# Performance work log

Hardware: AMD Instinct MI355X
Metric: run time of the kernel (lower is better)

The kernel has to match this reference:

```python
import jax, jax.numpy as jnp
import numpy as np

N_NODES = 100000
N_EDGES = 1600000
D_IN = 512
D_HID = 128
N_CLASSES = 100


def _gcn_norm(edge_index, n_nodes):
    # Add self loops and compute symmetric normalization D^{-1/2} (A+I) D^{-1/2}
    sl = jnp.arange(n_nodes, dtype=edge_index.dtype)
    src = jnp.concatenate([edge_index[0], sl])
    dst = jnp.concatenate([edge_index[1], sl])
    deg = jax.ops.segment_sum(jnp.ones_like(dst, dtype=jnp.float32), dst,
                              num_segments=n_nodes)
    dinv = jnp.where(deg > 0, jax.lax.rsqrt(deg), 0.0)
    norm = dinv[src] * dinv[dst]  # [E + N]
    return src, dst, norm


def _gcn_layer(x, W, b, src, dst, norm, n_nodes):
    h = x @ W                                  # [N, d_out] (transform first, like PyG GCNConv)
    msg = h[src] * norm[:, None]               # [E+N, d_out] gather + scale
    out = jax.ops.segment_sum(msg, dst, num_segments=n_nodes)  # scatter-add
    return out + b


def setup_inputs() -> dict:
    key = jax.random.key(0)
    ks = jax.random.split(key, 6)
    x = jax.random.normal(ks[0], (N_NODES, D_IN), dtype=jnp.float32)
    edge_index = jax.random.randint(ks[1], (2, N_EDGES), 0, N_NODES, dtype=jnp.int64)
    W1 = jax.random.normal(ks[2], (D_IN, D_HID), dtype=jnp.float32) * (1.0 / np.sqrt(D_IN))
    b1 = jnp.zeros((D_HID,), dtype=jnp.float32)
    W2 = jax.random.normal(ks[3], (D_HID, N_CLASSES), dtype=jnp.float32) * (1.0 / np.sqrt(D_HID))
    b2 = jnp.zeros((N_CLASSES,), dtype=jnp.float32)
    return {"x": x, "edge_index": edge_index, "W1": W1, "b1": b1, "W2": W2, "b2": b2}


def reference(x, edge_index, W1, b1, W2, b2):
    n_nodes = x.shape[0]
    src, dst, norm = _gcn_norm(edge_index, n_nodes)
    h = jax.nn.relu(_gcn_layer(x, W1, b1, src, dst, norm, n_nodes))
    logits = _gcn_layer(h, W2, b2, src, dst, norm, n_nodes)
    return jax.nn.log_softmax(logits, axis=-1)
```

## Files before the change

### kernel.cpp

```cpp
#include <hip/hip_runtime.h>
#include <math.h>

typedef __attribute__((ext_vector_type(8))) short short8;
typedef __attribute__((ext_vector_type(4))) float f32x4;
typedef _Float16 half8 __attribute__((ext_vector_type(8)));
typedef __fp16 fp16x2 __attribute__((ext_vector_type(2)));
typedef unsigned int uint;

__device__ inline uint f2bf(float f) {
    uint u = __float_as_uint(f);
    return (u + 0x7fffu + ((u >> 16) & 1u)) >> 16;
}
__device__ inline uint pack2(float lo, float hi) { return f2bf(lo) | (f2bf(hi) << 16); }
__device__ inline float bflo(uint u) { return __uint_as_float(u << 16); }
__device__ inline float bfhi(uint u) { return __uint_as_float(u & 0xffff0000u); }
__device__ inline uint cvtpk(float lo, float hi) {
    uint r;
    asm("v_cvt_pk_bf16_f32 %0, %1, %2" : "=v"(r) : "v"(lo), "v"(hi));
    return r;
}
__device__ inline uint pkh(float lo, float hi) {
    union { fp16x2 h; uint u; } c;
    c.h = __builtin_amdgcn_cvt_pkrtz(lo, hi);
    return c.u;
}
__device__ inline void gload16(const void* g, void* l) {
    __builtin_amdgcn_global_load_lds(
        (const __attribute__((address_space(1))) void*)g,
        (__attribute__((address_space(3))) void*)l, 16, 0, 0);
}

__global__ void k_prep(const int* __restrict__ dst, int E, int nbE, int* __restrict__ cnt,
                       const float* __restrict__ W1, ushort* __restrict__ w1frag,
                       const float* __restrict__ W2, const float* __restrict__ b2,
                       ushort* __restrict__ w2frag, float* __restrict__ b2pad) {
    int bid = blockIdx.x;
    if (bid < nbE) {
        int i = bid * 256 + threadIdx.x;
        if (i < E) atomicAdd(&cnt[dst[i]], 1);
        return;
    }
    bid -= nbE;
    if (bid < 32) {
        int tid = bid * 256 + threadIdx.x;
        int ks = tid >> 9;
        int t = (tid >> 6) & 7;
        int l = tid & 63;
        int kbase = ks * 32 + (l >> 4) * 8;
        int c = t * 16 + (l & 15);
#pragma unroll
        for (int j = 0; j < 8; j++) {
            float v = W1[(size_t)(kbase + j) * 128 + c];
            union { _Float16 h; ushort u; } cv;
            cv.h = (_Float16)v;
            w1frag[(size_t)tid * 8 + j] = cv.u;
        }
        return;
    }
    bid -= 32;
    {
        int tid = bid * 256 + threadIdx.x;
        if (tid < 1792) {
            int q = tid / 448;
            int t = (tid >> 6) % 7;
            int l = tid & 63;
            int kbase = q * 32 + (l >> 4) * 8;
            int c = t * 16 + (l & 15);
#pragma unroll
            for (int j = 0; j < 8; j++) {
                float v = (c < 100) ? W2[(kbase + j) * 100 + c] : 0.f;
                w2frag[(size_t)tid * 8 + j] = (ushort)f2bf(v);
            }
        } else if (tid < 1792 + 112) {
            int c = tid - 1792;
            b2pad[c] = (c < 100) ? b2[c] : -1e30f;
        }
    }
}

__global__ __launch_bounds__(512) void k_scan1(const int* __restrict__ cnt, int* __restrict__ rp,
                                               int* __restrict__ partials, float* __restrict__ dinv,
                                               int N) {
    __shared__ int s[512];
    int i = blockIdx.x * 512 + threadIdx.x;
    int v = (i < N) ? cnt[i] : 0;
    if (i < N) dinv[i] = rsqrtf((float)(v + 1));
    s[threadIdx.x] = v;
    __syncthreads();
    for (int d = 1; d < 512; d <<= 1) {
        int t = (threadIdx.x >= d) ? s[threadIdx.x - d] : 0;
        __syncthreads();
        s[threadIdx.x] += t;
        __syncthreads();
    }
    if (i < N) rp[i] = s[threadIdx.x] - v;
    if (threadIdx.x == 511) partials[blockIdx.x] = s[511];
}

__global__ __launch_bounds__(512) void k_scan3(int* __restrict__ rp, const int* __restrict__ partials,
                                               int N, int E) {
    __shared__ int sw[8];
    int bid = blockIdx.x, tid = threadIdx.x;
    int acc = 0;
    for (int i = tid; i < bid; i += 512) acc += partials[i];
#pragma unroll
    for (int d = 32; d > 0; d >>= 1) acc += __shfl_xor(acc, d, 64);
    if ((tid & 63) == 0) sw[tid >> 6] = acc;
    __syncthreads();
    int tot = 0;
#pragma unroll
    for (int w = 0; w < 8; w++) tot += sw[w];
    int i = bid * 512 + tid;
    if (i < N) rp[i] += tot;
    if (i == 0) rp[N] = E;
}

__global__ __launch_bounds__(512) void k_fillgemm1(const int* __restrict__ src, const int* __restrict__ dst,
                                                   int E, int nbF, const int* __restrict__ rp,
                                                   int* __restrict__ cursor, const float* __restrict__ dinv,
                                                   float2* __restrict__ colw,
                                                   const float* __restrict__ x,
                                                   const uint4* __restrict__ w1f,
                                                   uint* __restrict__ h1, int N) {
    __shared__ __align__(16) char lds[49152];
    if (blockIdx.x < nbF) {
        int i = blockIdx.x * 512 + threadIdx.x;
        if (i < E) {
            int d = dst[i];
            int s = src[i];
            int pos = rp[d] + atomicAdd(&cursor[d], 1);
            colw[pos] = make_float2(__int_as_float(s), dinv[s]);
        }
        return;
    }
    int tid = threadIdx.x, wv = tid >> 6, l = tid & 63;
    int cl = l & 15, kg = l >> 4;
    int row0 = (blockIdx.x - nbF) * 64;
    int rq = wv & 3, chalf = wv >> 2;

    int xr = tid >> 3, xs = tid & 7;
    int xrg = row0 + xr; if (xrg >= N) xrg = N - 1;
    const float* xsrc = x + (size_t)xrg * 512 + xs * 8;

    auto stageB = [&](int c) {
        char* bbase = lds + 16384 + (c & 1) * 16384;
        const char* bsrc = (const char*)w1f + (size_t)c * 16384;
#pragma unroll
        for (int i = 0; i < 2; i++) {
            int s = i * 512 + tid;
            gload16(bsrc + (size_t)s * 16, bbase + (size_t)(s - l) * 16);
        }
    };

    float4 f0, f1;
    auto loadx = [&](int c) {
        const float* p = xsrc + c * 64;
        f0 = *(const float4*)p;
        f1 = *(const float4*)(p + 4);
    };
    auto writex = [&](int c) {
        char* xb = lds + (c & 1) * 8192;
        uint4 v;
        v.x = pkh(f0.x, f0.y);
        v.y = pkh(f0.z, f0.w);
        v.z = pkh(f1.x, f1.y);
        v.w = pkh(f1.z, f1.w);
        *(uint4*)(xb + xr * 128 + ((xs ^ (xr & 7)) * 16)) = v;
    };

    f32x4 acc[4];
#pragma unroll
    for (int t = 0; t < 4; t++) acc[t] = (f32x4){0.f, 0.f, 0.f, 0.f};

    union U { uint4 u4; half8 h8; };
    int arow = rq * 16 + cl;

    loadx(0);
    stageB(0);
    writex(0);
    __syncthreads();

    for (int c = 0; c < 8; c++) {
        if (c < 7) { loadx(c + 1); stageB(c + 1); }
        const char* xb = lds + (c & 1) * 8192;
        const char* bb = lds + 16384 + (c & 1) * 16384;
#pragma unroll
        for (int k2 = 0; k2 < 2; k2++) {
            U A;
            A.u4 = *(const uint4*)(xb + arow * 128 + (((k2 * 4 + kg) ^ (arow & 7)) * 16));
#pragma unroll
            for (int tt = 0; tt < 4; tt++) {
                U B;
                B.u4 = *(const uint4*)(bb + (size_t)(((k2 * 8 + chalf * 4 + tt) * 64 + l)) * 16);
                acc[tt] = __builtin_amdgcn_mfma_f32_16x16x32_f16(A.h8, B.h8, acc[tt], 0, 0, 0);
            }
        }
        if (c < 7) writex(c + 1);
        __syncthreads();
    }

    uint* hsp = (uint*)lds + (size_t)wv * (16 * 33);
#pragma unroll
    for (int tt = 0; tt < 4; tt++)
#pragma unroll
        for (int r = 0; r < 4; r++) {
            float mine = acc[tt][r];
            float other = __shfl_xor(mine, 1, 64);
            if ((cl & 1) == 0)
                hsp[(kg * 4 + r) * 33 + tt * 8 + (cl >> 1)] = cvtpk(mine, other);
        }
#pragma unroll
    for (int p = 0; p < 8; p++) {
        int it = p * 2 + (l >> 5);
        int gr = row0 + rq * 16 + it;
        if (gr < N) h1[(size_t)gr * 64 + chalf * 32 + (l & 31)] = hsp[it * 33 + (l & 31)];
    }
}

template <bool RELU_BIAS>
__global__ __launch_bounds__(256) void k_agg(const uint* __restrict__ h, const float* __restrict__ dinv,
                                             const int* __restrict__ rp, const float2* __restrict__ colw,
                                             const float* __restrict__ bias, uint* __restrict__ outb, int N) {
    int wave = threadIdx.x >> 6, lane = threadIdx.x & 63;
    int v = blockIdx.x * 4 + wave;
    if (v >= N) return;
    float dv = dinv[v];
    float wself = dv * dv;
    uint us = h[(size_t)v * 64 + lane];
    float acc0 = bflo(us) * wself;
    float acc1 = bfhi(us) * wself;
    int e0 = rp[v], e1 = rp[v + 1];
    int i = e0;
    for (; i + 8 <= e1; i += 8) {
        float2 q[8];
        uint u[8];
#pragma unroll
        for (int j = 0; j < 8; j++) q[j] = colw[i + j];
#pragma unroll
        for (int j = 0; j < 8; j++) u[j] = h[(size_t)__float_as_int(q[j].x) * 64 + lane];
#pragma unroll
        for (int j = 0; j < 8; j++) {
            float w = q[j].y * dv;
            acc0 = fmaf(bflo(u[j]), w, acc0);
            acc1 = fmaf(bfhi(u[j]), w, acc1);
        }
    }
    if (i + 4 <= e1) {
        float2 q[4];
        uint u[4];
#pragma unroll
        for (int j = 0; j < 4; j++) q[j] = colw[i + j];
#pragma unroll
        for (int j = 0; j < 4; j++) u[j] = h[(size_t)__float_as_int(q[j].x) * 64 + lane];
#pragma unroll
        for (int j = 0; j < 4; j++) {
            float w = q[j].y * dv;
            acc0 = fmaf(bflo(u[j]), w, acc0);
            acc1 = fmaf(bfhi(u[j]), w, acc1);
        }
        i += 4;
    }
    for (; i < e1; i++) {
        float2 q = colw[i];
        uint u = h[(size_t)__float_as_int(q.x) * 64 + lane];
        float w = q.y * dv;
        acc0 = fmaf(bflo(u), w, acc0);
        acc1 = fmaf(bfhi(u), w, acc1);
    }
    if (RELU_BIAS) {
        float2 b = *(const float2*)&bias[2 * lane];
        acc0 = fmaxf(acc0 + b.x, 0.f);
        acc1 = fmaxf(acc1 + b.y, 0.f);
    }
    outb[(size_t)v * 64 + lane] = pack2(acc0, acc1);
}

__global__ __launch_bounds__(256) void k_out_mfma(const uint* __restrict__ g2u,
                                                  const uint4* __restrict__ w2fragG,
                                                  const float* __restrict__ b2pad,
                                                  float* __restrict__ out, int N) {
    __shared__ uint4 w2s[1792];
    __shared__ float b2s[112];
    int tid = threadIdx.x;
    for (int i = tid; i < 1792; i += 256) w2s[i] = w2fragG[i];
    if (tid < 112) b2s[tid] = b2pad[tid];
    __syncthreads();

    int w = tid >> 6, l = tid & 63;
    int v0 = blockIdx.x * 128 + w * 32;
    int cl = l & 15, gq = l >> 4;

    f32x4 acc[2][7];
#pragma unroll
    for (int m = 0; m < 2; m++)
#pragma unroll
        for (int t = 0; t < 7; t++) acc[m][t] = (f32x4){0.f, 0.f, 0.f, 0.f};

    union U { uint4 u4; short8 s8; };

#pragma unroll
    for (int q = 0; q < 4; q++) {
        short8 afr[2];
#pragma unroll
        for (int m = 0; m < 2; m++) {
            int rv = v0 + m * 16 + cl;
            if (rv >= N) rv = N - 1;
            U a;
            a.u4 = *(const uint4*)&g2u[(size_t)rv * 64 + q * 16 + gq * 4];
            afr[m] = a.s8;
        }
#pragma unroll
        for (int t = 0; t < 7; t++) {
            U b;
            b.u4 = w2s[(q * 7 + t) * 64 + l];
            acc[0][t] = __builtin_amdgcn_mfma_f32_16x16x32_bf16(afr[0], b.s8, acc[0][t], 0, 0, 0);
            acc[1][t] = __builtin_amdgcn_mfma_f32_16x16x32_bf16(afr[1], b.s8, acc[1][t], 0, 0, 0);
        }
    }

    float bsv[7];
#pragma unroll
    for (int t = 0; t < 7; t++) bsv[t] = b2s[t * 16 + cl];

#pragma unroll
    for (int m = 0; m < 2; m++) {
#pragma unroll
        for (int r = 0; r < 4; r++) {
            int row = v0 + m * 16 + gq * 4 + r;
            float lg[7];
#pragma unroll
            for (int t = 0; t < 7; t++) lg[t] = acc[m][t][r] + bsv[t];
            float mx = lg[0];
#pragma unroll
            for (int t = 1; t < 7; t++) mx = fmaxf(mx, lg[t]);
            mx = fmaxf(mx, __shfl_xor(mx, 1, 64));
            mx = fmaxf(mx, __shfl_xor(mx, 2, 64));
            mx = fmaxf(mx, __shfl_xor(mx, 4, 64));
            mx = fmaxf(mx, __shfl_xor(mx, 8, 64));
            float s = 0.f;
#pragma unroll
            for (int t = 0; t < 7; t++) s += __expf(lg[t] - mx);
            s += __shfl_xor(s, 1, 64);
            s += __shfl_xor(s, 2, 64);
            s += __shfl_xor(s, 4, 64);
            s += __shfl_xor(s, 8, 64);
            float lse = mx + __logf(s);
            if (row < N) {
#pragma unroll
                for (int t = 0; t < 7; t++) {
                    int c = t * 16 + cl;
                    if (c < 100) out[(size_t)row * 100 + c] = lg[t] - lse;
                }
            }
        }
    }
}

extern "C" void kernel_launch(void* const* d_in, const int* in_sizes, int n_in,
                              void* d_out, int out_size, void* d_ws, size_t ws_size,
                              hipStream_t stream) {
    const float* x  = (const float*)d_in[0];
    const int*   ei = (const int*)d_in[1];
    const float* W1 = (const float*)d_in[2];
    const float* b1 = (const float*)d_in[3];
    const float* W2 = (const float*)d_in[4];
    const float* b2 = (const float*)d_in[5];
    float* out = (float*)d_out;

    int N = in_sizes[0] / 512;
    int E = in_sizes[1] / 2;
    const int* srcI = ei;
    const int* dstI = ei + E;

    char* wsb = (char*)d_ws;
    size_t off = 0;
    auto alloc = [&](size_t bytes) {
        void* p = wsb + off;
        off = (off + bytes + 255) & ~(size_t)255;
        return p;
    };
    int*    cnt      = (int*)alloc((size_t)N * 4);
    int*    cursor   = (int*)alloc((size_t)N * 4);
    float*  dinv     = (float*)alloc((size_t)N * 4);
    int*    rp       = (int*)alloc((size_t)(N + 1) * 4);
    int*    partials = (int*)alloc(1024 * 4);
    ushort* w1f      = (ushort*)alloc(8192 * 8 * 2);
    ushort* w2frag   = (ushort*)alloc(1792 * 8 * 2);
    float*  b2pad    = (float*)alloc(112 * 4);
    float2* colw     = (float2*)alloc((size_t)E * 8);
    uint*   h1       = (uint*)alloc((size_t)N * 64 * 4);
    uint*   a1       = (uint*)alloc((size_t)N * 64 * 4);
    uint*   g2       = h1;

    hipMemsetAsync(cnt, 0, (size_t)2 * (((size_t)N * 4 + 255) & ~(size_t)255), stream);

    int nbE = (E + 255) / 256;
    k_prep<<<nbE + 40, 256, 0, stream>>>(dstI, E, nbE, cnt, W1, w1f, W2, b2, w2frag, b2pad);
    int nb = (N + 511) / 512;
    k_scan1<<<nb, 512, 0, stream>>>(cnt, rp, partials, dinv, N);
    k_scan3<<<nb, 512, 0, stream>>>(rp, partials, N, E);

    int nbF = (E + 511) / 512;
    int nbG = (N + 63) / 64;
    k_fillgemm1<<<nbF + nbG, 512, 0, stream>>>(srcI, dstI, E, nbF, rp, cursor, dinv, colw,
                                               x, (const uint4*)w1f, h1, N);

    k_agg<true><<<(N + 3) / 4, 256, 0, stream>>>(h1, dinv, rp, colw, b1, a1, N);
    k_agg<false><<<(N + 3) / 4, 256, 0, stream>>>(a1, dinv, rp, colw, nullptr, g2, N);
    k_out_mfma<<<(N + 127) / 128, 256, 0, stream>>>(g2, (const uint4*)w2frag, b2pad, out, N);
}
```

Baseline: 367.1 us.

## Split fill from GEMM1 and load whole x tile into LDS at once

Separates the CSR fill and the first GEMM into two kernels. The GEMM now loads the full 64x512 x tile into a 64KB LDS buffer up front, instead of double-buffering it in chunks, and streams W1 fragments straight from global into registers with one-step prefetch instead of staging them through LDS. The aim is fewer barriers and more memory requests in flight. The costs are an extra kernel launch, lost overlap between fill and GEMM, and lower occupancy from 64KB of LDS and 16 float4 registers per thread.

Result: slower. 379.2 us (+3.3%).

```diff
diff --git a/kernel.cpp b/kernel.cpp
--- a/kernel.cpp
+++ b/kernel.cpp
@@ -23,11 +23,6 @@
     union { fp16x2 h; uint u; } c;
     c.h = __builtin_amdgcn_cvt_pkrtz(lo, hi);
     return c.u;
-}
-__device__ inline void gload16(const void* g, void* l) {
-    __builtin_amdgcn_global_load_lds(
-        (const __attribute__((address_space(1))) void*)g,
-        (__attribute__((address_space(3))) void*)l, 16, 0, 0);
 }
 
 __global__ void k_prep(const int* __restrict__ dst, int E, int nbE, int* __restrict__ cnt,
@@ -115,58 +110,45 @@
     if (i == 0) rp[N] = E;
 }
 
-__global__ __launch_bounds__(512) void k_fillgemm1(const int* __restrict__ src, const int* __restrict__ dst,
-                                                   int E, int nbF, const int* __restrict__ rp,
-                                                   int* __restrict__ cursor, const float* __restrict__ dinv,
-                                                   float2* __restrict__ colw,
-                                                   const float* __restrict__ x,
-                                                   const uint4* __restrict__ w1f,
-                                                   uint* __restrict__ h1, int N) {
-    __shared__ __align__(16) char lds[49152];
-    if (blockIdx.x < nbF) {
-        int i = blockIdx.x * 512 + threadIdx.x;
-        if (i < E) {
-            int d = dst[i];
-            int s = src[i];
-            int pos = rp[d] + atomicAdd(&cursor[d], 1);
-            colw[pos] = make_float2(__int_as_float(s), dinv[s]);
-        }
-        return;
-    }
+__global__ void k_fill(const int* __restrict__ src, const int* __restrict__ dst, int E,
+                       const int* __restrict__ rp, int* __restrict__ cursor,
+                       const float* __restrict__ dinv, float2* __restrict__ colw) {
+    int i = blockIdx.x * 256 + threadIdx.x;
+    if (i < E) {
+        int d = dst[i];
+        int s = src[i];
+        int pos = rp[d] + atomicAdd(&cursor[d], 1);
+        colw[pos] = make_float2(__int_as_float(s), dinv[s]);
+    }
+}
+
+__global__ __launch_bounds__(512) void k_gemm1(const float* __restrict__ x,
+                                               const uint4* __restrict__ w1f,
+                                               uint* __restrict__ h1, int N) {
+    __shared__ __align__(16) char lds[65536];
     int tid = threadIdx.x, wv = tid >> 6, l = tid & 63;
     int cl = l & 15, kg = l >> 4;
-    int row0 = (blockIdx.x - nbF) * 64;
+    int row0 = blockIdx.x * 64;
     int rq = wv & 3, chalf = wv >> 2;
 
-    int xr = tid >> 3, xs = tid & 7;
-    int xrg = row0 + xr; if (xrg >= N) xrg = N - 1;
-    const float* xsrc = x + (size_t)xrg * 512 + xs * 8;
-
-    auto stageB = [&](int c) {
-        char* bbase = lds + 16384 + (c & 1) * 16384;
-        const char* bsrc = (const char*)w1f + (size_t)c * 16384;
-#pragma unroll
-        for (int i = 0; i < 2; i++) {
-            int s = i * 512 + tid;
-            gload16(bsrc + (size_t)s * 16, bbase + (size_t)(s - l) * 16);
-        }
-    };
-
-    float4 f0, f1;
-    auto loadx = [&](int c) {
-        const float* p = xsrc + c * 64;
-        f0 = *(const float4*)p;
-        f1 = *(const float4*)(p + 4);
-    };
-    auto writex = [&](int c) {
-        char* xb = lds + (c & 1) * 8192;
-        uint4 v;
-        v.x = pkh(f0.x, f0.y);
-        v.y = pkh(f0.z, f0.w);
-        v.z = pkh(f1.x, f1.y);
-        v.w = pkh(f1.z, f1.w);
-        *(uint4*)(xb + xr * 128 + ((xs ^ (xr & 7)) * 16)) = v;
-    };
+    float4 xa[16];
+#pragma unroll
+    for (int p = 0; p < 16; p++) {
+        int g4 = p * 512 + tid;
+        int r = g4 >> 7;
+        int rg = row0 + r; if (rg >= N) rg = N - 1;
+        xa[p] = *(const float4*)(x + (size_t)rg * 512 + (size_t)(g4 & 127) * 4);
+    }
+#pragma unroll
+    for (int p = 0; p < 16; p++) {
+        int g4 = p * 512 + tid;
+        int r = g4 >> 7;
+        int f = g4 & 127;
+        int gran = (f >> 1) ^ (r & 7);
+        *(uint2*)(lds + (size_t)r * 1024 + gran * 16 + (f & 1) * 8)
+            = make_uint2(pkh(xa[p].x, xa[p].y), pkh(xa[p].z, xa[p].w));
+    }
+    __syncthreads();
 
     f32x4 acc[4];
 #pragma unroll
@@ -174,30 +156,34 @@
 
     union U { uint4 u4; half8 h8; };
     int arow = rq * 16 + cl;
-
-    loadx(0);
-    stageB(0);
-    writex(0);
-    __syncthreads();
-
-    for (int c = 0; c < 8; c++) {
-        if (c < 7) { loadx(c + 1); stageB(c + 1); }
-        const char* xb = lds + (c & 1) * 8192;
-        const char* bb = lds + 16384 + (c & 1) * 16384;
-#pragma unroll
-        for (int k2 = 0; k2 < 2; k2++) {
-            U A;
-            A.u4 = *(const uint4*)(xb + arow * 128 + (((k2 * 4 + kg) ^ (arow & 7)) * 16));
-#pragma unroll
-            for (int tt = 0; tt < 4; tt++) {
-                U B;
-                B.u4 = *(const uint4*)(bb + (size_t)(((k2 * 8 + chalf * 4 + tt) * 64 + l)) * 16);
-                acc[tt] = __builtin_amdgcn_mfma_f32_16x16x32_f16(A.h8, B.h8, acc[tt], 0, 0, 0);
-            }
-        }
-        if (c < 7) writex(c + 1);
-        __syncthreads();
-    }
+    const char* xrow = lds + (size_t)arow * 1024;
+    int sw = arow & 7;
+
+    uint4 bq[4];
+#pragma unroll
+    for (int tt = 0; tt < 4; tt++) bq[tt] = w1f[(chalf * 4 + tt) * 64 + l];
+
+    for (int ks = 0; ks < 16; ks++) {
+        U A;
+        A.u4 = *(const uint4*)(xrow + (((ks * 4 + kg) ^ sw) * 16));
+        uint4 bn[4];
+        if (ks < 15) {
+#pragma unroll
+            for (int tt = 0; tt < 4; tt++)
+                bn[tt] = w1f[((ks + 1) * 8 + chalf * 4 + tt) * 64 + l];
+        }
+#pragma unroll
+        for (int tt = 0; tt < 4; tt++) {
+            U B;
+            B.u4 = bq[tt];
+            acc[tt] = __builtin_amdgcn_mfma_f32_16x16x32_f16(A.h8, B.h8, acc[tt], 0, 0, 0);
+        }
+        if (ks < 15) {
+#pragma unroll
+            for (int tt = 0; tt < 4; tt++) bq[tt] = bn[tt];
+        }
+    }
+    __syncthreads();
 
     uint* hsp = (uint*)lds + (size_t)wv * (16 * 33);
 #pragma unroll
@@ -399,12 +385,9 @@
     int nb = (N + 511) / 512;
     k_scan1<<<nb, 512, 0, stream>>>(cnt, rp, partials, dinv, N);
     k_scan3<<<nb, 512, 0, stream>>>(rp, partials, N, E);
-
-    int nbF = (E + 511) / 512;
-    int nbG = (N + 63) / 64;
-    k_fillgemm1<<<nbF + nbG, 512, 0, stream>>>(srcI, dstI, E, nbF, rp, cursor, dinv, colw,
-                                               x, (const uint4*)w1f, h1, N);
-
+    k_fill<<<(E + 255) / 256, 256, 0, stream>>>(srcI, dstI, E, rp, cursor, dinv, colw);
+
+    k_gemm1<<<(N + 63) / 64, 512, 0, stream>>>(x, (const uint4*)w1f, h1, N);
     k_agg<true><<<(N + 3) / 4, 256, 0, stream>>>(h1, dinv, rp, colw, b1, a1, N);
     k_agg<false><<<(N + 3) / 4, 256, 0, stream>>>(a1, dinv, rp, colw, nullptr, g2, N);
     k_out_mfma<<<(N + 127) / 128, 256, 0, stream>>>(g2, (const uint4*)w2frag, b2pad, out, N);
```
